# Performance work log

Hardware: AMD Instinct MI355X
Metric: run time of the kernel (lower is better)

## Reference

```python
import jax, jax.numpy as jnp
import numpy as np

Q, L = 512, 4096


def setup_inputs() -> dict:
    key = jax.random.key(0)
    ks = jax.random.split(key, 12)
    def rn(k, shape, s=0.05):
        return jax.random.normal(k, shape, jnp.float32) * s
    return {
        "reactions": jax.random.normal(ks[0], (1, Q, 256), jnp.float32),
        "protein":   jax.random.normal(ks[1], (1, L, 1024), jnp.float32),
        # conv1d(1024->256, k=1) == pointwise linear
        "Wc":  rn(ks[2], (256, 1024)), "bc":  jnp.zeros((256,), jnp.float32),
        "W1":  rn(ks[3], (64, 256)),   "b1":  jnp.zeros((64,), jnp.float32),
        "W2":  rn(ks[4], (64, 256)),   "b2":  jnp.zeros((64,), jnp.float32),
        "Wa":  rn(ks[5], (64, 64)),    "ba":  jnp.zeros((64,), jnp.float32),
        "Wpa": rn(ks[6], (64, 64)),    "bpa": jnp.zeros((64,), jnp.float32),
        "Wra": rn(ks[7], (64, 64)),    "bra": jnp.zeros((64,), jnp.float32),
        "Wf1": rn(ks[8], (256, 128)),  "bf1": jnp.zeros((256,), jnp.float32),
        "Wf2": rn(ks[9], (128, 256)),  "bf2": jnp.zeros((128,), jnp.float32),
        "Wf3": rn(ks[10], (1, 128)),   "bf3": jnp.zeros((1,), jnp.float32),
    }


def reference(reactions, protein, Wc, bc, W1, b1, W2, b2, Wa, ba,
              Wpa, bpa, Wra, bra, Wf1, bf1, Wf2, bf2, Wf3, bf3):
    # protein: [1, L, 1024] -> 1x1 conv over channels == linear -> [L, 256]
    p = jax.nn.relu(protein[0] @ Wc.T + bc)
    # reactions: [1, Q, 256] -> [Q, 64]
    r = jax.nn.relu(reactions[0] @ W2.T + b2)
    # protein tokens -> [L, 64]
    k = jax.nn.relu(p @ W1.T + b1)

    ra = r @ Wra.T + bra            # [Q, 64]
    pa = k @ Wpa.T + bpa            # [L, 64]
    # broadcast outer-sum + relu + small linear: [Q, L, 64]
    A = jax.nn.relu(ra[:, None, :] + pa[None, :, :]) @ Wa.T + ba

    r_gate = jax.nn.sigmoid(jnp.mean(A, axis=1))   # [Q, 64]
    p_gate = jax.nn.sigmoid(jnp.mean(A, axis=0))   # [L, 64]

    rxnfp = r + r * r_gate                          # [Q, 64]
    prot = jnp.max(k + k * p_gate, axis=0)          # [64]  maxpool over L

    ctx = jnp.concatenate(
        [rxnfp, jnp.broadcast_to(prot, (rxnfp.shape[0], 64))], axis=1)  # [Q,128]

    # dropout layers are identity in eval mode
    h = jax.nn.leaky_relu(ctx @ Wf1.T + bf1)
    h = jax.nn.leaky_relu(h @ Wf2.T + bf2)
    out = h @ Wf3.T + bf3
    return out.reshape(-1)                          # [Q]
```

## Files before the change

### kernel.cpp

```cpp
#include <hip/hip_runtime.h>
#include <hip/hip_bf16.h>
#include <math.h>

#define TPB 256

typedef __attribute__((ext_vector_type(8))) short s16x8;
typedef __attribute__((ext_vector_type(4))) float f32x4;

#define MFMA16(a, b, c) __builtin_amdgcn_mfma_f32_16x16x32_bf16((a), (b), (c), 0, 0, 0)

constexpr unsigned OFF_P    = 0u;
constexpr unsigned OFF_K    = OFF_P    + 4096u*256u;
constexpr unsigned OFF_PA   = OFF_K    + 4096u*64u;
constexpr unsigned OFF_R    = OFF_PA   + 4096u*64u;
constexpr unsigned OFF_RA   = OFF_R    + 512u*64u;
constexpr unsigned OFF_SR   = OFF_RA   + 512u*64u;
constexpr unsigned OFF_PMAX = OFF_SR   + 512u*64u;
constexpr unsigned OFF_SP   = OFF_PMAX + 64u;

__device__ __forceinline__ short f2bf(float x) {
  union { float f; unsigned u; } v; v.f = x;
  unsigned r = v.u + 0x7FFFu + ((v.u >> 16) & 1u);
  return (short)(r >> 16);
}
__device__ __forceinline__ unsigned pkbf(float a, float b) {
  __hip_bfloat162 h = __float22bfloat162_rn(make_float2(a, b));
  union { __hip_bfloat162 h2; unsigned u; } v; v.h2 = h;
  return v.u;
}
union U8 { s16x8 s; unsigned u[4]; };

__global__ __launch_bounds__(TPB, 2) void k1_gemm(
    const float* __restrict__ prot, const float* __restrict__ Wc,
    const float* __restrict__ bc,   float* __restrict__ ws)
{
  int bid = blockIdx.x;
  int tid = threadIdx.x;
  if (bid >= 512) {
    if (tid < 16)
      *(float4*)&ws[OFF_PMAX + tid * 4] = make_float4(0.f, 0.f, 0.f, 0.f);
    return;
  }

  __shared__ __align__(16) short Asm[32 * 72];
  __shared__ __align__(16) short Bsm[64 * 72];

  int m0 = (bid >> 2) * 32;
  int n0 = (bid & 3) * 64;
  int wave = tid >> 6, lane = tid & 63;
  int wm = (wave & 1) * 16, wn = (wave >> 1) * 32;
  int lm = lane & 15, quad = lane >> 4;

  int arow = tid >> 3, aseg = (tid & 7) * 8;
  int brow = tid >> 2, bseg = (tid & 3) * 16;

  const float* Ag = prot + (size_t)(m0 + arow) * 1024 + aseg;
  const float* Bg = Wc   + (size_t)(n0 + brow) * 1024 + bseg;

  float4 a4[2], b4[4];
#pragma unroll
  for (int i = 0; i < 2; ++i) a4[i] = *(const float4*)(Ag + i * 4);
#pragma unroll
  for (int i = 0; i < 4; ++i) b4[i] = *(const float4*)(Bg + i * 4);

  f32x4 acc[2] = {};

  for (int kc = 0; kc < 16; ++kc) {
    __syncthreads();
    {
      U8 s;
      s.u[0] = pkbf(a4[0].x, a4[0].y); s.u[1] = pkbf(a4[0].z, a4[0].w);
      s.u[2] = pkbf(a4[1].x, a4[1].y); s.u[3] = pkbf(a4[1].z, a4[1].w);
      *(s16x8*)&Asm[arow * 72 + aseg] = s.s;
    }
#pragma unroll
    for (int h = 0; h < 2; ++h) {
      U8 s;
      s.u[0] = pkbf(b4[h*2].x,   b4[h*2].y);
      s.u[1] = pkbf(b4[h*2].z,   b4[h*2].w);
      s.u[2] = pkbf(b4[h*2+1].x, b4[h*2+1].y);
      s.u[3] = pkbf(b4[h*2+1].z, b4[h*2+1].w);
      *(s16x8*)&Bsm[brow * 72 + bseg + h * 8] = s.s;
    }
    if (kc < 15) {
#pragma unroll
      for (int i = 0; i < 2; ++i) a4[i] = *(const float4*)(Ag + (kc + 1) * 64 + i * 4);
#pragma unroll
      for (int i = 0; i < 4; ++i) b4[i] = *(const float4*)(Bg + (kc + 1) * 64 + i * 4);
    }
    __syncthreads();
#pragma unroll
    for (int ks = 0; ks < 2; ++ks) {
      s16x8 af = *(const s16x8*)&Asm[(wm + lm) * 72 + ks * 32 + quad * 8];
#pragma unroll
      for (int ni = 0; ni < 2; ++ni) {
        s16x8 bfv = *(const s16x8*)&Bsm[(wn + ni * 16 + lm) * 72 + ks * 32 + quad * 8];
        acc[ni] = MFMA16(af, bfv, acc[ni]);
      }
    }
  }

#pragma unroll
  for (int ni = 0; ni < 2; ++ni) {
    int col = n0 + wn + ni * 16 + lm;
    float bcv = bc[col];
#pragma unroll
    for (int r = 0; r < 4; ++r) {
      int row = m0 + wm + quad * 4 + r;
      ws[OFF_P + (unsigned)row * 256u + col] = fmaxf(acc[ni][r] + bcv, 0.f);
    }
  }
}

__global__ __launch_bounds__(TPB, 2) void k2_heads(
    const float* __restrict__ reactions,
    const float* __restrict__ W1,  const float* __restrict__ b1,
    const float* __restrict__ W2,  const float* __restrict__ b2,
    const float* __restrict__ Wpa, const float* __restrict__ bpa,
    const float* __restrict__ Wra, const float* __restrict__ bra,
    float* __restrict__ ws)
{
  __shared__ __align__(16) short Asm[32 * 264];
  __shared__ __align__(16) short Bsm[64 * 264];
  __shared__ __align__(16) short Ksm[32 * 72];
  __shared__ __align__(16) short Wsm[64 * 72];
  int bid = blockIdx.x, tid = threadIdx.x;
  bool isProt = bid < 128;
  int row0 = (isProt ? bid : (bid - 128)) * 32;
  const float* src  = isProt ? (ws + OFF_P) : reactions;
  const float* Wst1 = isProt ? W1 : W2;
  const float* bv   = isProt ? b1 : b2;
  const float* Wst2 = isProt ? Wpa : Wra;
  const float* b2nd = isProt ? bpa : bra;
  float* out1 = ws + (isProt ? OFF_K : OFF_R);
  float* out2 = ws + (isProt ? OFF_PA : OFF_RA);

  {
    int row = tid >> 3, seg = (tid & 7) * 32;
    const float* sp = src + (size_t)(row0 + row) * 256 + seg;
    float4 f[8];
#pragma unroll
    for (int i = 0; i < 8; ++i) f[i] = *(const float4*)(sp + i * 4);
#pragma unroll
    for (int i = 0; i < 4; ++i) {
      U8 s;
      s.u[0] = pkbf(f[2*i].x,   f[2*i].y);
      s.u[1] = pkbf(f[2*i].z,   f[2*i].w);
      s.u[2] = pkbf(f[2*i+1].x, f[2*i+1].y);
      s.u[3] = pkbf(f[2*i+1].z, f[2*i+1].w);
      *(s16x8*)&Asm[row * 264 + seg + i * 8] = s.s;
    }
  }
  {
    int row = tid >> 2, seg = (tid & 3) * 64;
    const float* sp = Wst1 + (size_t)row * 256 + seg;
#pragma unroll
    for (int i = 0; i < 8; ++i) {
      float4 fa = *(const float4*)(sp + i * 8);
      float4 fb = *(const float4*)(sp + i * 8 + 4);
      U8 s;
      s.u[0] = pkbf(fa.x, fa.y); s.u[1] = pkbf(fa.z, fa.w);
      s.u[2] = pkbf(fb.x, fb.y); s.u[3] = pkbf(fb.z, fb.w);
      *(s16x8*)&Bsm[row * 264 + seg + i * 8] = s.s;
    }
  }
  {
    int row = tid >> 2, seg = (tid & 3) * 16;
    const float* sp = Wst2 + (size_t)row * 64 + seg;
#pragma unroll
    for (int i = 0; i < 2; ++i) {
      float4 fa = *(const float4*)(sp + i * 8);
      float4 fb = *(const float4*)(sp + i * 8 + 4);
      U8 s;
      s.u[0] = pkbf(fa.x, fa.y); s.u[1] = pkbf(fa.z, fa.w);
      s.u[2] = pkbf(fb.x, fb.y); s.u[3] = pkbf(fb.z, fb.w);
      *(s16x8*)&Wsm[row * 72 + seg + i * 8] = s.s;
    }
  }
  __syncthreads();

  int wave = tid >> 6, lane = tid & 63;
  int lm = lane & 15, quad = lane >> 4;
  int wm = (wave >> 1) * 16, wn = (wave & 1) * 32;

  f32x4 acc[2] = {};
#pragma unroll
  for (int kc = 0; kc < 8; ++kc) {
    s16x8 a = *(const s16x8*)&Asm[(wm + lm) * 264 + kc * 32 + quad * 8];
#pragma unroll
    for (int ni = 0; ni < 2; ++ni) {
      s16x8 b = *(const s16x8*)&Bsm[(wn + ni * 16 + lm) * 264 + kc * 32 + quad * 8];
      acc[ni] = MFMA16(a, b, acc[ni]);
    }
  }
#pragma unroll
  for (int ni = 0; ni < 2; ++ni) {
    int col = wn + ni * 16 + lm;
    float bb = bv[col];
#pragma unroll
    for (int r = 0; r < 4; ++r) {
      int row = wm + quad * 4 + r;
      float kv = fmaxf(acc[ni][r] + bb, 0.f);
      out1[(size_t)(row0 + row) * 64 + col] = kv;
      Ksm[row * 72 + col] = f2bf(kv);
    }
  }
  __syncthreads();

  f32x4 acc2[2] = {};
#pragma unroll
  for (int kc = 0; kc < 2; ++kc) {
    s16x8 a = *(const s16x8*)&Ksm[(wm + lm) * 72 + kc * 32 + quad * 8];
#pragma unroll
    for (int ni = 0; ni < 2; ++ni) {
      s16x8 b = *(const s16x8*)&Wsm[(wn + ni * 16 + lm) * 72 + kc * 32 + quad * 8];
      acc2[ni] = MFMA16(a, b, acc2[ni]);
    }
  }
#pragma unroll
  for (int ni = 0; ni < 2; ++ni) {
    int col = wn + ni * 16 + lm;
    float bb = b2nd[col];
#pragma unroll
    for (int r = 0; r < 4; ++r) {
      int row = wm + quad * 4 + r;
      out2[(size_t)(row0 + row) * 64 + col] = acc2[ni][r] + bb;
    }
  }
}

__global__ __launch_bounds__(TPB) void k3h_hist(float* __restrict__ ws)
{
  __shared__ float xcol[4096];
  __shared__ float rcol[512];
  __shared__ float hc[1025];
  __shared__ float hs[1025];
  __shared__ float rmn[4], rmx[4];
  int c = blockIdx.x, tid = threadIdx.x;
  int wave = tid >> 6, lane = tid & 63;
  const float* pa = ws + OFF_PA;
  const float* ra = ws + OFF_RA;

  for (int i = tid; i < 4096; i += TPB) xcol[i] = pa[(unsigned)i * 64u + c];
  for (int i = tid; i < 512;  i += TPB) rcol[i] = ra[(unsigned)i * 64u + c];
  for (int i = tid; i < 1025; i += TPB) { hc[i] = 0.f; hs[i] = 0.f; }
  __syncthreads();

  float mn = 1e30f, mx = -1e30f;
  for (int i = tid; i < 4096; i += TPB) {
    float x = xcol[i];
    mn = fminf(mn, x); mx = fmaxf(mx, x);
  }
#pragma unroll
  for (int off = 32; off > 0; off >>= 1) {
    mn = fminf(mn, __shfl_down(mn, off));
    mx = fmaxf(mx, __shfl_down(mx, off));
  }
  if (lane == 0) { rmn[wave] = mn; rmx[wave] = mx; }
  __syncthreads();
  mn = fminf(fminf(rmn[0], rmn[1]), fminf(rmn[2], rmn[3]));
  mx = fmaxf(fmaxf(rmx[0], rmx[1]), fmaxf(rmx[2], rmx[3]));
  float w = (mx - mn) * (1.f / 1024.f);
  float invw = (w > 1e-30f) ? 1.f / w : 0.f;
  for (int i = tid; i < 4096; i += TPB) {
    float x = xcol[i];
    int b = (int)((x - mn) * invw);
    b = b < 0 ? 0 : (b > 1023 ? 1023 : b);
    atomicAdd(&hc[b], 1.f);
    atomicAdd(&hs[b], x);
  }
  __syncthreads();
  if (wave == 0) {
    float vc[16], vs[16], sc = 0.f, ss = 0.f;
#pragma unroll
    for (int i = 0; i < 16; ++i) {
      vc[i] = hc[lane * 16 + i]; sc += vc[i];
      vs[i] = hs[lane * 16 + i]; ss += vs[i];
    }
    float tc = sc, ts = ss;
#pragma unroll
    for (int off = 1; off < 64; off <<= 1) {
      float oc = __shfl_down(tc, off);
      float os = __shfl_down(ts, off);
      if (lane + off < 64) { tc += oc; ts += os; }
    }
    float runc = tc - sc, runs = ts - ss;
#pragma unroll
    for (int i = 15; i >= 0; --i) {
      runc += vc[i]; hc[lane * 16 + i] = runc;
      runs += vs[i]; hs[lane * 16 + i] = runs;
    }
  }
  __syncthreads();
  for (int q = tid; q < 512; q += TPB) {
    float u = rcol[q];
    float thr = -u;
    int b;
    if (thr < mn) b = 0;
    else { b = (int)((thr - mn) * invw) + 1; b = b > 1024 ? 1024 : b; }
    ws[OFF_SR + (unsigned)q * 64u + c] = u * hc[b] + hs[b];
  }
  __syncthreads();

  for (int i = tid; i < 1025; i += TPB) { hc[i] = 0.f; hs[i] = 0.f; }
  float mn2 = 1e30f, mx2 = -1e30f;
  for (int i = tid; i < 512; i += TPB) {
    float x = rcol[i];
    mn2 = fminf(mn2, x); mx2 = fmaxf(mx2, x);
  }
#pragma unroll
  for (int off = 32; off > 0; off >>= 1) {
    mn2 = fminf(mn2, __shfl_down(mn2, off));
    mx2 = fmaxf(mx2, __shfl_down(mx2, off));
  }
  __syncthreads();
  if (lane == 0) { rmn[wave] = mn2; rmx[wave] = mx2; }
  __syncthreads();
  mn2 = fminf(fminf(rmn[0], rmn[1]), fminf(rmn[2], rmn[3]));
  mx2 = fmaxf(fmaxf(rmx[0], rmx[1]), fmaxf(rmx[2], rmx[3]));
  float w2 = (mx2 - mn2) * (1.f / 1024.f);
  float invw2 = (w2 > 1e-30f) ? 1.f / w2 : 0.f;
  for (int i = tid; i < 512; i += TPB) {
    float x = rcol[i];
    int b = (int)((x - mn2) * invw2);
    b = b < 0 ? 0 : (b > 1023 ? 1023 : b);
    atomicAdd(&hc[b], 1.f);
    atomicAdd(&hs[b], x);
  }
  __syncthreads();
  if (wave == 0) {
    float vc[16], vs[16], sc = 0.f, ss = 0.f;
#pragma unroll
    for (int i = 0; i < 16; ++i) {
      vc[i] = hc[lane * 16 + i]; sc += vc[i];
      vs[i] = hs[lane * 16 + i]; ss += vs[i];
    }
    float tc = sc, ts = ss;
#pragma unroll
    for (int off = 1; off < 64; off <<= 1) {
      float oc = __shfl_down(tc, off);
      float os = __shfl_down(ts, off);
      if (lane + off < 64) { tc += oc; ts += os; }
    }
    float runc = tc - sc, runs = ts - ss;
#pragma unroll
    for (int i = 15; i >= 0; --i) {
      runc += vc[i]; hc[lane * 16 + i] = runc;
      runs += vs[i]; hs[lane * 16 + i] = runs;
    }
  }
  __syncthreads();
  for (int l = tid; l < 4096; l += TPB) {
    float v = xcol[l];
    float thr = -v;
    int b;
    if (thr < mn2) b = 0;
    else { b = (int)((thr - mn2) * invw2) + 1; b = b > 1024 ? 1024 : b; }
    ws[OFF_SP + (unsigned)l * 64u + c] = v * hc[b] + hs[b];
  }
}

__global__ __launch_bounds__(TPB) void k3b_gate(
    const float* __restrict__ Wa, const float* __restrict__ ba,
    float* __restrict__ ws)
{
  __shared__ float sp[16 * 64];
  __shared__ float wat[64 * 65];
  int bid = blockIdx.x, tid = threadIdx.x;
  int c = tid & 63, g = tid >> 6;
  int l0 = bid * 16;
  {
    int idx = tid * 4;
    float4 v = *(const float4*)&ws[OFF_SP + (unsigned)l0 * 64u + idx];
    v.x *= (1.f / 512.f); v.y *= (1.f / 512.f);
    v.z *= (1.f / 512.f); v.w *= (1.f / 512.f);
    *(float4*)&sp[idx] = v;
  }
  for (int it = 0; it < 16; ++it) {
    int idx = it * TPB + tid;
    wat[(idx & 63) * 65 + (idx >> 6)] = Wa[idx];
  }
  __syncthreads();
  float vmax = 0.f;
  float bac = ba[c];
#pragma unroll
  for (int i = 0; i < 4; ++i) {
    int ll = g * 4 + i;
    float dot = 0.f;
#pragma unroll 8
    for (int jj = 0; jj < 64; ++jj)
      dot += sp[ll * 64 + jj] * wat[jj * 65 + c];
    float pg = 1.f / (1.f + __expf(-(dot + bac)));
    float val = ws[OFF_K + (unsigned)(l0 + ll) * 64u + c] * (1.f + pg);
    vmax = fmaxf(vmax, val);
  }
  atomicMax((int*)&ws[OFF_PMAX + c], __float_as_int(vmax));
}

__global__ __launch_bounds__(TPB) void k4_final(
    const float* __restrict__ Wa,  const float* __restrict__ ba,
    const float* __restrict__ Wf1, const float* __restrict__ bf1,
    const float* __restrict__ Wf2, const float* __restrict__ bf2,
    const float* __restrict__ Wf3, const float* __restrict__ bf3,
    float* __restrict__ ws, float* __restrict__ out)
{
  __shared__ __align__(16) short mrb[16 * 72];
  __shared__ __align__(16) short wab[64 * 72];
  __shared__ __align__(16) short ctxb[16 * 136];
  __shared__ __align__(16) short h1b[16 * 264];
  __shared__ __align__(16) short wgt[256 * 136];
  __shared__ float red[64];
  int bid = blockIdx.x, tid = threadIdx.x;
  int q0 = bid * 16;
  int wave = tid >> 6, lane = tid & 63;
  int lm = lane & 15, quad = lane >> 4;

  {
    int q = tid >> 4, c4 = (tid & 15) * 4;
    float4 v = *(const float4*)&ws[OFF_SR + (unsigned)(q0 + q) * 64u + c4];
    uint2 st = make_uint2(pkbf(v.x * (1.f/4096.f), v.y * (1.f/4096.f)),
                          pkbf(v.z * (1.f/4096.f), v.w * (1.f/4096.f)));
    *(uint2*)&mrb[q * 72 + c4] = st;
  }
#pragma unroll
  for (int it = 0; it < 4; ++it) {
    int i4 = it * TPB + tid;
    int row = i4 >> 4, c4 = (i4 & 15) * 4;
    float4 v = *(const float4*)&Wa[row * 64 + c4];
    uint2 st = make_uint2(pkbf(v.x, v.y), pkbf(v.z, v.w));
    *(uint2*)&wab[row * 72 + c4] = st;
  }
  __syncthreads();

  f32x4 gacc = {};
#pragma unroll
  for (int kc = 0; kc < 2; ++kc) {
    s16x8 a = *(const s16x8*)&mrb[lm * 72 + kc * 32 + quad * 8];
    s16x8 b = *(const s16x8*)&wab[(wave * 16 + lm) * 72 + kc * 32 + quad * 8];
    gacc = MFMA16(a, b, gacc);
  }
  {
    int c = wave * 16 + lm;
    float bac = ba[c];
    short pb = f2bf(ws[OFF_PMAX + c]);
#pragma unroll
    for (int r = 0; r < 4; ++r) {
      int q = quad * 4 + r;
      float gg = 1.f / (1.f + __expf(-(gacc[r] + bac)));
      float rv = ws[OFF_R + (unsigned)(q0 + q) * 64u + c];
      ctxb[q * 136 + c]      = f2bf(rv * (1.f + gg));
      ctxb[q * 136 + 64 + c] = pb;
    }
  }
#pragma unroll 4
  for (int it = 0; it < 32; ++it) {
    int i4 = it * TPB + tid;
    int row = i4 >> 5, c4 = (i4 & 31) * 4;
    float4 v = *(const float4*)&Wf1[row * 128 + c4];
    uint2 st = make_uint2(pkbf(v.x, v.y), pkbf(v.z, v.w));
    *(uint2*)&wgt[row * 136 + c4] = st;
  }
  __syncthreads();

  f32x4 h[4] = {};
#pragma unroll
  for (int kc = 0; kc < 4; ++kc) {
    s16x8 a = *(const s16x8*)&ctxb[lm * 136 + kc * 32 + quad * 8];
#pragma unroll
    for (int nt = 0; nt < 4; ++nt) {
      s16x8 b = *(const s16x8*)&wgt[(wave * 64 + nt * 16 + lm) * 136 + kc * 32 + quad * 8];
      h[nt] = MFMA16(a, b, h[nt]);
    }
  }
#pragma unroll
  for (int nt = 0; nt < 4; ++nt) {
    int n = wave * 64 + nt * 16 + lm;
    float bb = bf1[n];
#pragma unroll
    for (int r = 0; r < 4; ++r) {
      int q = quad * 4 + r;
      float v = h[nt][r] + bb;
      v = v > 0.f ? v : 0.01f * v;
      h1b[q * 264 + n] = f2bf(v);
    }
  }
  __syncthreads();

#pragma unroll 4
  for (int it = 0; it < 32; ++it) {
    int i4 = it * TPB + tid;
    int row = i4 >> 6, c4 = (i4 & 63) * 4;
    float4 v = *(const float4*)&Wf2[row * 256 + c4];
    uint2 st = make_uint2(pkbf(v.x, v.y), pkbf(v.z, v.w));
    *(uint2*)&wgt[row * 264 + c4] = st;
  }
  __syncthreads();

  f32x4 o[2] = {};
#pragma unroll
  for (int kc = 0; kc < 8; ++kc) {
    s16x8 a = *(const s16x8*)&h1b[lm * 264 + kc * 32 + quad * 8];
#pragma unroll
    for (int nt = 0; nt < 2; ++nt) {
      s16x8 b = *(const s16x8*)&wgt[(wave * 32 + nt * 16 + lm) * 264 + kc * 32 + quad * 8];
      o[nt] = MFMA16(a, b, o[nt]);
    }
  }
  float pv[4] = {0.f, 0.f, 0.f, 0.f};
#pragma unroll
  for (int nt = 0; nt < 2; ++nt) {
    int m = wave * 32 + nt * 16 + lm;
    float bb = bf2[m], w3 = Wf3[m];
#pragma unroll
    for (int r = 0; r < 4; ++r) {
      float v = o[nt][r] + bb;
      v = v > 0.f ? v : 0.01f * v;
      pv[r] += v * w3;
    }
  }
#pragma unroll
  for (int msk = 1; msk < 16; msk <<= 1)
#pragma unroll
    for (int r = 0; r < 4; ++r) pv[r] += __shfl_xor(pv[r], msk);
  if (lm == 0) {
#pragma unroll
    for (int r = 0; r < 4; ++r) red[(quad * 4 + r) * 4 + wave] = pv[r];
  }
  __syncthreads();
  if (tid < 16)
    out[q0 + tid] = red[tid * 4] + red[tid * 4 + 1] + red[tid * 4 + 2] +
                    red[tid * 4 + 3] + bf3[0];
}

extern "C" void kernel_launch(void* const* d_in, const int* in_sizes, int n_in,
                              void* d_out, int out_size, void* d_ws, size_t ws_size,
                              hipStream_t stream)
{
  const float* reactions = (const float*)d_in[0];
  const float* protein   = (const float*)d_in[1];
  const float* Wc  = (const float*)d_in[2];
  const float* bc  = (const float*)d_in[3];
  const float* W1  = (const float*)d_in[4];
  const float* b1  = (const float*)d_in[5];
  const float* W2  = (const float*)d_in[6];
  const float* b2  = (const float*)d_in[7];
  const float* Wa  = (const float*)d_in[8];
  const float* ba  = (const float*)d_in[9];
  const float* Wpa = (const float*)d_in[10];
  const float* bpa = (const float*)d_in[11];
  const float* Wra = (const float*)d_in[12];
  const float* bra = (const float*)d_in[13];
  const float* Wf1 = (const float*)d_in[14];
  const float* bf1 = (const float*)d_in[15];
  const float* Wf2 = (const float*)d_in[16];
  const float* bf2 = (const float*)d_in[17];
  const float* Wf3 = (const float*)d_in[18];
  const float* bf3 = (const float*)d_in[19];
  float* ws  = (float*)d_ws;
  float* out = (float*)d_out;

  hipLaunchKernelGGL(k1_gemm, dim3(513), dim3(TPB), 0, stream,
                     protein, Wc, bc, ws);
  hipLaunchKernelGGL(k2_heads, dim3(144), dim3(TPB), 0, stream,
                     reactions, W1, b1, W2, b2, Wpa, bpa, Wra, bra, ws);
  hipLaunchKernelGGL(k3h_hist, dim3(64), dim3(TPB), 0, stream, ws);
  hipLaunchKernelGGL(k3b_gate, dim3(256), dim3(TPB), 0, stream, Wa, ba, ws);
  hipLaunchKernelGGL(k4_final, dim3(32), dim3(TPB), 0, stream,
                     Wa, ba, Wf1, bf1, Wf2, bf2, Wf3, bf3, ws, out);
}
```

Baseline: 178.5 us.

## Split histogram passes across blocks and read transposed pa/ra columns

The histogram kernel is launched with twice as many blocks, so each channel's two passes (protein histogram for the reaction sums, reaction histogram for the protein sums) run in separate blocks instead of one after the other. The heads kernel also writes pa and ra in transposed column-major form, so the histogram kernel can load each channel column with contiguous float4 reads rather than strided scalar reads. This adds extra scattered global stores in k2_heads and more workspace memory.

Result: faster. 170.0 us (-4.8%).

```diff
diff --git a/kernel.cpp b/kernel.cpp
--- a/kernel.cpp
+++ b/kernel.cpp
@@ -17,6 +17,8 @@
 constexpr unsigned OFF_SR   = OFF_RA   + 512u*64u;
 constexpr unsigned OFF_PMAX = OFF_SR   + 512u*64u;
 constexpr unsigned OFF_SP   = OFF_PMAX + 64u;
+constexpr unsigned OFF_PAT  = OFF_SP   + 4096u*64u;
+constexpr unsigned OFF_RAT  = OFF_PAT  + 64u*4096u;
 
 __device__ __forceinline__ short f2bf(float x) {
   union { float f; unsigned u; } v; v.f = x;
@@ -132,8 +134,10 @@
   const float* bv   = isProt ? b1 : b2;
   const float* Wst2 = isProt ? Wpa : Wra;
   const float* b2nd = isProt ? bpa : bra;
-  float* out1 = ws + (isProt ? OFF_K : OFF_R);
-  float* out2 = ws + (isProt ? OFF_PA : OFF_RA);
+  float* out1  = ws + (isProt ? OFF_K : OFF_R);
+  float* out2  = ws + (isProt ? OFF_PA : OFF_RA);
+  float* out2T = ws + (isProt ? OFF_PAT : OFF_RAT);
+  unsigned tstride = isProt ? 4096u : 512u;
 
   {
     int row = tid >> 3, seg = (tid & 7) * 32;
@@ -224,7 +228,9 @@
 #pragma unroll
     for (int r = 0; r < 4; ++r) {
       int row = wm + quad * 4 + r;
-      out2[(size_t)(row0 + row) * 64 + col] = acc2[ni][r] + bb;
+      float v = acc2[ni][r] + bb;
+      out2[(size_t)(row0 + row) * 64 + col] = v;
+      out2T[(size_t)col * tstride + (row0 + row)] = v;
     }
   }
 }
@@ -236,19 +242,25 @@
   __shared__ float hc[1025];
   __shared__ float hs[1025];
   __shared__ float rmn[4], rmx[4];
-  int c = blockIdx.x, tid = threadIdx.x;
+  int bid = blockIdx.x, tid = threadIdx.x;
   int wave = tid >> 6, lane = tid & 63;
-  const float* pa = ws + OFF_PA;
-  const float* ra = ws + OFF_RA;
-
-  for (int i = tid; i < 4096; i += TPB) xcol[i] = pa[(unsigned)i * 64u + c];
-  for (int i = tid; i < 512;  i += TPB) rcol[i] = ra[(unsigned)i * 64u + c];
+  bool passA = bid < 64;
+  int c = passA ? bid : (bid - 64);
+  const float* paT = ws + OFF_PAT + (size_t)c * 4096;
+  const float* raT = ws + OFF_RAT + (size_t)c * 512;
+
+  for (int i = tid * 4; i < 4096; i += TPB * 4)
+    *(float4*)&xcol[i] = *(const float4*)(paT + i);
+  if (tid * 4 < 512)
+    *(float4*)&rcol[tid * 4] = *(const float4*)(raT + tid * 4);
   for (int i = tid; i < 1025; i += TPB) { hc[i] = 0.f; hs[i] = 0.f; }
   __syncthreads();
 
+  const float* hsrc = passA ? xcol : rcol;
+  int hn = passA ? 4096 : 512;
   float mn = 1e30f, mx = -1e30f;
-  for (int i = tid; i < 4096; i += TPB) {
-    float x = xcol[i];
+  for (int i = tid; i < hn; i += TPB) {
+    float x = hsrc[i];
     mn = fminf(mn, x); mx = fmaxf(mx, x);
   }
 #pragma unroll
@@ -262,8 +274,8 @@
   mx = fmaxf(fmaxf(rmx[0], rmx[1]), fmaxf(rmx[2], rmx[3]));
   float w = (mx - mn) * (1.f / 1024.f);
   float invw = (w > 1e-30f) ? 1.f / w : 0.f;
-  for (int i = tid; i < 4096; i += TPB) {
-    float x = xcol[i];
+  for (int i = tid; i < hn; i += TPB) {
+    float x = hsrc[i];
     int b = (int)((x - mn) * invw);
     b = b < 0 ? 0 : (b > 1023 ? 1023 : b);
     atomicAdd(&hc[b], 1.f);
@@ -292,71 +304,25 @@
     }
   }
   __syncthreads();
-  for (int q = tid; q < 512; q += TPB) {
-    float u = rcol[q];
-    float thr = -u;
-    int b;
-    if (thr < mn) b = 0;
-    else { b = (int)((thr - mn) * invw) + 1; b = b > 1024 ? 1024 : b; }
-    ws[OFF_SR + (unsigned)q * 64u + c] = u * hc[b] + hs[b];
-  }
-  __syncthreads();
-
-  for (int i = tid; i < 1025; i += TPB) { hc[i] = 0.f; hs[i] = 0.f; }
-  float mn2 = 1e30f, mx2 = -1e30f;
-  for (int i = tid; i < 512; i += TPB) {
-    float x = rcol[i];
-    mn2 = fminf(mn2, x); mx2 = fmaxf(mx2, x);
-  }
-#pragma unroll
-  for (int off = 32; off > 0; off >>= 1) {
-    mn2 = fminf(mn2, __shfl_down(mn2, off));
-    mx2 = fmaxf(mx2, __shfl_down(mx2, off));
-  }
-  __syncthreads();
-  if (lane == 0) { rmn[wave] = mn2; rmx[wave] = mx2; }
-  __syncthreads();
-  mn2 = fminf(fminf(rmn[0], rmn[1]), fminf(rmn[2], rmn[3]));
-  mx2 = fmaxf(fmaxf(rmx[0], rmx[1]), fmaxf(rmx[2], rmx[3]));
-  float w2 = (mx2 - mn2) * (1.f / 1024.f);
-  float invw2 = (w2 > 1e-30f) ? 1.f / w2 : 0.f;
-  for (int i = tid; i < 512; i += TPB) {
-    float x = rcol[i];
-    int b = (int)((x - mn2) * invw2);
-    b = b < 0 ? 0 : (b > 1023 ? 1023 : b);
-    atomicAdd(&hc[b], 1.f);
-    atomicAdd(&hs[b], x);
-  }
-  __syncthreads();
-  if (wave == 0) {
-    float vc[16], vs[16], sc = 0.f, ss = 0.f;
-#pragma unroll
-    for (int i = 0; i < 16; ++i) {
-      vc[i] = hc[lane * 16 + i]; sc += vc[i];
-      vs[i] = hs[lane * 16 + i]; ss += vs[i];
-    }
-    float tc = sc, ts = ss;
-#pragma unroll
-    for (int off = 1; off < 64; off <<= 1) {
-      float oc = __shfl_down(tc, off);
-      float os = __shfl_down(ts, off);
-      if (lane + off < 64) { tc += oc; ts += os; }
-    }
-    float runc = tc - sc, runs = ts - ss;
-#pragma unroll
-    for (int i = 15; i >= 0; --i) {
-      runc += vc[i]; hc[lane * 16 + i] = runc;
-      runs += vs[i]; hs[lane * 16 + i] = runs;
-    }
-  }
-  __syncthreads();
-  for (int l = tid; l < 4096; l += TPB) {
-    float v = xcol[l];
-    float thr = -v;
-    int b;
-    if (thr < mn2) b = 0;
-    else { b = (int)((thr - mn2) * invw2) + 1; b = b > 1024 ? 1024 : b; }
-    ws[OFF_SP + (unsigned)l * 64u + c] = v * hc[b] + hs[b];
+
+  if (passA) {
+    for (int q = tid; q < 512; q += TPB) {
+      float u = rcol[q];
+      float thr = -u;
+      int b;
+      if (thr < mn) b = 0;
+      else { b = (int)((thr - mn) * invw) + 1; b = b > 1024 ? 1024 : b; }
+      ws[OFF_SR + (unsigned)q * 64u + c] = u * hc[b] + hs[b];
+    }
+  } else {
+    for (int l = tid; l < 4096; l += TPB) {
+      float v = xcol[l];
+      float thr = -v;
+      int b;
+      if (thr < mn) b = 0;
+      else { b = (int)((thr - mn) * invw) + 1; b = b > 1024 ? 1024 : b; }
+      ws[OFF_SP + (unsigned)l * 64u + c] = v * hc[b] + hs[b];
+    }
   }
 }
 
@@ -563,7 +529,7 @@
                      protein, Wc, bc, ws);
   hipLaunchKernelGGL(k2_heads, dim3(144), dim3(TPB), 0, stream,
                      reactions, W1, b1, W2, b2, Wpa, bpa, Wra, bra, ws);
-  hipLaunchKernelGGL(k3h_hist, dim3(64), dim3(TPB), 0, stream, ws);
+  hipLaunchKernelGGL(k3h_hist, dim3(128), dim3(TPB), 0, stream, ws);
   hipLaunchKernelGGL(k3b_gate, dim3(256), dim3(TPB), 0, stream, Wa, ba, ws);
   hipLaunchKernelGGL(k4_final, dim3(32), dim3(TPB), 0, stream,
                      Wa, ba, Wf1, bf1, Wf2, bf2, Wf3, bf3, ws, out);
```
